# Kernel optimization log

Hardware: AMD Instinct MI355X
Metric: run time of the kernel (lower is better)

The kernel has to match this reference:

```python
import jax, jax.numpy as jnp
import numpy as np

H, DH, DM = 8, 128, 1024          # n_head, d_head, d_model (n_head*d_head == d_model)
SLEN, BSZ = 256, 64               # slen <= 256 forced by pi0[:, :l]
SCALE = 1.0 / DH ** 0.5
LN_EPS = 1e-5


def setup_inputs() -> dict:
    key = jax.random.key(0)
    k0, k1, k2, k3 = jax.random.split(key, 4)
    h = jax.random.normal(k0, (SLEN, BSZ, DM), jnp.float32)
    W_qkv = jax.random.normal(k1, (H * 4 * DH, DM), jnp.float32) * (DM ** -0.5)
    W_o = jax.random.normal(k2, (DM, H * DH), jnp.float32) * ((H * DH) ** -0.5)
    pi0 = jax.random.uniform(k3, (H, 256), jnp.float32)
    ln_gamma = jnp.ones((DM,), jnp.float32)
    ln_beta = jnp.zeros((DM,), jnp.float32)
    return {"h": h, "W_qkv": W_qkv, "W_o": W_o, "pi0": pi0,
            "ln_gamma": ln_gamma, "ln_beta": ln_beta}


def _phi(x):
    # elu(x)+1 feature map, then L1-normalize over the feature dim
    x = jax.nn.elu(x) + 1.0
    return x / jnp.sum(x, axis=-1, keepdims=True)


def _causal_linear_attn(q, k, v):
    # fast_weight_sum: out_t = sum_{s<=t} (q_t . k_s) v_s  (zero initial fast weights)
    # q,k,v: [b,h,l,d]
    l = q.shape[2]
    scores = jnp.einsum('bhld,bhsd->bhls', q, k)
    mask = jnp.tril(jnp.ones((l, l), dtype=bool))
    scores = jnp.where(mask, scores, jnp.zeros((), scores.dtype))
    return jnp.einsum('bhls,bhsd->bhld', scores, v)


def reference(h, W_qkv, W_o, pi0, ln_gamma, ln_beta):
    l, b, _ = h.shape
    # qkv projection: [l,b,H,4*DH] -> q, k1, k2, v (update_mode='rbf2keys')
    qkv = jnp.einsum('lbm,nm->lbn', h, W_qkv).reshape(l, b, H, 4 * DH)
    q, k1, k2, v = jnp.split(qkv, 4, axis=-1)
    # permute to [b, H, l, d]
    q = _phi(jnp.transpose(q, (1, 2, 0, 3)))
    k1 = _phi(jnp.transpose(k1, (1, 2, 0, 3)))
    k2 = _phi(jnp.transpose(k2, (1, 2, 0, 3)))
    v = jnp.transpose(v, (1, 2, 0, 3))
    # two fast-weight sums (skip_attn_normalization=True path)
    lo1 = _causal_linear_attn(q, k1, v)
    lo2 = _causal_linear_attn(q, k2, v)
    pi = jnp.clip(pi0, 0.0, 1.0)[None, :, :l, None]          # [1,H,l,1]
    layer_out = SCALE * (lo1 * pi + lo2 * (1.0 - pi))         # [b,H,l,d]
    # [b,H,l,d] -> [l,b,H*d]
    layer_out = jnp.transpose(layer_out, (2, 0, 1, 3)).reshape(l, b, H * DH)
    attn_out = jnp.einsum('lbn,mn->lbm', layer_out, W_o)
    # post-LN residual (pre_lnorm=False, dropout=0)
    x = h + attn_out
    mu = jnp.mean(x, axis=-1, keepdims=True)
    var = jnp.mean((x - mu) ** 2, axis=-1, keepdims=True)
    return ln_gamma * (x - mu) / jnp.sqrt(var + LN_EPS) + ln_beta
```

## Files before the change

kernel.cpp:

```cpp
#include <hip/hip_runtime.h>

#define H_     8
#define DM_    1024
#define NQKV_  4096
#define ROWS_  16384
#define PAIRS_ 512
#define SCALE_ 0.08838834764831845f
#define LN_EPS_ 1e-5f

typedef __attribute__((ext_vector_type(8))) short short8;
typedef __attribute__((ext_vector_type(4))) short short4v;
typedef __attribute__((ext_vector_type(4))) float floatx4;

__device__ __forceinline__ float b2f(unsigned short u) {
  union { unsigned int i; float f; } v; v.i = ((unsigned int)u) << 16; return v.f;
}
__device__ __forceinline__ unsigned short f2b(float f) {
  union { unsigned int i; float f; } v; v.f = f;
  unsigned int b = v.i;
  b += 0x7FFFu + ((b >> 16) & 1u);
  return (unsigned short)(b >> 16);
}

__device__ __forceinline__ void gl_lds(const unsigned short* g, unsigned short* s) {
  __builtin_amdgcn_global_load_lds(
      (const __attribute__((address_space(1))) unsigned int*)g,
      (__attribute__((address_space(3))) unsigned int*)s, 16, 0, 0);
}

__device__ __forceinline__ void stage_async(const unsigned short* __restrict__ g,
                                            size_t ld, unsigned short* s, int tid) {
#pragma unroll
  for (int p = 0; p < 4; ++p) {
    int idx = p * 256 + tid;
    int r = idx >> 3, j = idx & 7;
    int cg = j ^ (r & 7);
    gl_lds(g + (size_t)r * ld + cg * 8, s + (size_t)idx * 8);
  }
}
__device__ __forceinline__ void stage_h(const unsigned short* __restrict__ g,
                                        size_t o0, size_t o1,
                                        unsigned short* s, int lo0, int lo1) {
  gl_lds(g + o0, s + lo0);
  gl_lds(g + o1, s + lo1);
}
__device__ __forceinline__ short8 lds_frag(const unsigned short* s, int row, int cg) {
  return *(const short8*)(s + row * 64 + ((cg ^ (row & 7)) << 3));
}

__global__ __launch_bounds__(256) void cvt_all(const float* __restrict__ h,
                                               const float* __restrict__ wq,
                                               const float* __restrict__ wo,
                                               unsigned short* __restrict__ hb,
                                               unsigned short* __restrict__ wqb,
                                               unsigned short* __restrict__ wob) {
  int i = blockIdx.x * 256 + threadIdx.x;
  const float* src; unsigned short* dst; int off;
  if (i < 2097152)      { src = h;  dst = hb;  off = i; }
  else if (i < 2621440) { src = wq; dst = wqb; off = i - 2097152; }
  else                  { src = wo; dst = wob; off = i - 2621440; }
  const float4* s4 = (const float4*)(src + (size_t)off * 8);
  float4 v0 = s4[0], v1 = s4[1];
  union { short8 v; unsigned short u[8]; } pk;
  pk.u[0] = f2b(v0.x); pk.u[1] = f2b(v0.y); pk.u[2] = f2b(v0.z); pk.u[3] = f2b(v0.w);
  pk.u[4] = f2b(v1.x); pk.u[5] = f2b(v1.y); pk.u[6] = f2b(v1.z); pk.u[7] = f2b(v1.w);
  *(short8*)(dst + (size_t)off * 8) = pk.v;
}

__global__ __launch_bounds__(1024, 4) void qkv_gemm(const unsigned short* __restrict__ A,
                                                    const unsigned short* __restrict__ B,
                                                    unsigned short* __restrict__ QKV) {
  __shared__ alignas(16) unsigned short Sh[65536];
  int tid = threadIdx.x;
  int lane = tid & 63, wid = tid >> 6;
  int wm = wid >> 2, wn = wid & 3;
  int quad = lane >> 4, l16 = lane & 15;
  int s7 = l16 & 7;

  int bid = blockIdx.y * 16 + blockIdx.x;
  int swz = (bid & 7) * 128 + (bid >> 3);
  int bx = swz & 15, by = swz >> 4;
  int n0 = bx * 256, hh = bx >> 1, part0 = (bx & 1) * 2, bb = by;

  const unsigned short* AbP = A + (size_t)bb * DM_;
  const size_t lda = (size_t)64 * DM_;
  const unsigned short* BbP = B + (size_t)n0 * DM_;

  int r0 = tid >> 3, jj = tid & 7;
  int cg = jj ^ (r0 & 7);
  size_t oA = (size_t)r0 * lda + cg * 8;
  size_t oB = (size_t)r0 * DM_ + cg * 8;
  int lo = tid * 8;

  floatx4 acc[4][4];
#pragma unroll
  for (int i = 0; i < 4; ++i)
#pragma unroll
    for (int j = 0; j < 4; ++j)
#pragma unroll
      for (int r = 0; r < 4; ++r) acc[i][j][r] = 0.f;

#define QSTAGE(KT, SA)                                                         \
  gl_lds(AbP + (KT) + oA,                     (SA) + lo);                      \
  gl_lds(AbP + (KT) + oA + (size_t)128 * lda, (SA) + 8192 + lo);               \
  gl_lds(BbP + (KT) + oB,                     (SA) + 16384 + lo);              \
  gl_lds(BbP + (KT) + oB + (size_t)128 * DM_, (SA) + 24576 + lo);

  QSTAGE(0, Sh)

  for (int t = 0; t < 16; ++t) {
    unsigned short* SA = Sh + (t & 1) * 32768;
    if (t < 15) { QSTAGE((size_t)(t + 1) * 64, Sh + ((t + 1) & 1) * 32768) }
    if (t < 15) { asm volatile("s_waitcnt vmcnt(4)" ::: "memory"); }
    else        { asm volatile("s_waitcnt vmcnt(0)" ::: "memory"); }
    __builtin_amdgcn_s_barrier();
    const unsigned short* aB0 = SA + (wm * 64 + l16) * 64 + ((quad ^ s7) << 3);
    const unsigned short* aB1 = SA + (wm * 64 + l16) * 64 + (((4 + quad) ^ s7) << 3);
    const unsigned short* bB0 = SA + 16384 + (wn * 64 + l16) * 64 + ((quad ^ s7) << 3);
    const unsigned short* bB1 = SA + 16384 + (wn * 64 + l16) * 64 + (((4 + quad) ^ s7) << 3);
    short8 a[4], b[4];
#pragma unroll
    for (int mt = 0; mt < 4; ++mt) a[mt] = *(const short8*)(aB0 + mt * 1024);
#pragma unroll
    for (int nt = 0; nt < 4; ++nt) b[nt] = *(const short8*)(bB0 + nt * 1024);
#pragma unroll
    for (int mt = 0; mt < 4; ++mt)
#pragma unroll
      for (int nt = 0; nt < 4; ++nt)
        acc[mt][nt] = __builtin_amdgcn_mfma_f32_16x16x32_bf16(a[mt], b[nt], acc[mt][nt], 0, 0, 0);
#pragma unroll
    for (int mt = 0; mt < 4; ++mt) a[mt] = *(const short8*)(aB1 + mt * 1024);
#pragma unroll
    for (int nt = 0; nt < 4; ++nt) b[nt] = *(const short8*)(bB1 + nt * 1024);
#pragma unroll
    for (int mt = 0; mt < 4; ++mt)
#pragma unroll
      for (int nt = 0; nt < 4; ++nt)
        acc[mt][nt] = __builtin_amdgcn_mfma_f32_16x16x32_bf16(a[mt], b[nt], acc[mt][nt], 0, 0, 0);
    __builtin_amdgcn_s_barrier();
  }
#undef QSTAGE

  int c16 = tid & 15, g64 = tid >> 4;
  bool isV = (part0 + (wn >> 1)) == 3;
  float* Pf = (float*)Sh;
  float rsum[4][4], inv[4][4];
  if (!isV) {
#pragma unroll
    for (int mt = 0; mt < 4; ++mt)
#pragma unroll
      for (int r = 0; r < 4; ++r) rsum[mt][r] = 0.f;
#pragma unroll
    for (int mt = 0; mt < 4; ++mt)
#pragma unroll
      for (int nt = 0; nt < 4; ++nt)
#pragma unroll
        for (int r = 0; r < 4; ++r) {
          float x = acc[mt][nt][r];
          float f = x > 0.f ? x + 1.f : __expf(x);
          acc[mt][nt][r] = f;
          rsum[mt][r] += f;
        }
#pragma unroll
    for (int off = 1; off < 16; off <<= 1)
#pragma unroll
      for (int mt = 0; mt < 4; ++mt)
#pragma unroll
        for (int r = 0; r < 4; ++r)
          rsum[mt][r] += __shfl_xor(rsum[mt][r], off);
    if (l16 == 0) {
#pragma unroll
      for (int mt = 0; mt < 4; ++mt)
#pragma unroll
        for (int r = 0; r < 4; ++r)
          Pf[(wm * 64 + mt * 16 + quad * 4 + r) * 4 + wn] = rsum[mt][r];
    }
  }
  __syncthreads();
  if (!isV) {
#pragma unroll
    for (int mt = 0; mt < 4; ++mt)
#pragma unroll
      for (int r = 0; r < 4; ++r)
        inv[mt][r] = 1.f / (rsum[mt][r] + Pf[(wm * 64 + mt * 16 + quad * 4 + r) * 4 + (wn ^ 1)]);
  }
  __syncthreads();

#pragma unroll
  for (int hq = 0; hq < 2; ++hq) {
    int part = part0 + hq;
    if ((wn >> 1) == hq) {
      if (part < 3) {
#pragma unroll
        for (int mt = 0; mt < 4; ++mt)
#pragma unroll
          for (int nt = 0; nt < 4; ++nt)
#pragma unroll
            for (int r = 0; r < 4; ++r) {
              int row = wm * 64 + mt * 16 + quad * 4 + r;
              int col = (wn & 1) * 64 + nt * 16 + l16;
              Sh[row * 136 + col] = f2b(acc[mt][nt][r] * inv[mt][r]);
            }
      } else {
#pragma unroll
        for (int mt = 0; mt < 4; ++mt)
#pragma unroll
          for (int nt = 0; nt < 4; ++nt)
#pragma unroll
            for (int r = 0; r < 4; ++r) {
              int d = (wn & 1) * 64 + nt * 16 + l16;
              int l = wm * 64 + mt * 16 + quad * 4 + r;
              Sh[d * 264 + l] = f2b(acc[mt][nt][r]);
            }
      }
    }
    __syncthreads();
    if (part < 3) {
      unsigned short* P = QKV + (size_t)part * 16777216 + (size_t)(bb * 8 + hh) * 32768;
#pragma unroll
      for (int j = 0; j < 4; ++j) {
        int row = j * 64 + g64;
        *(short8*)(P + (size_t)row * 128 + c16 * 8) = *(const short8*)(Sh + row * 136 + c16 * 8);
      }
    } else {
      unsigned short* Vt = QKV + (size_t)3 * 16777216 + (size_t)(bb * 8 + hh) * 32768;
      int cg2 = tid & 31, g32 = tid >> 5;
#pragma unroll
      for (int j = 0; j < 4; ++j) {
        int d = j * 32 + g32;
        *(short8*)(Vt + (size_t)d * 256 + cg2 * 8) = *(const short8*)(Sh + d * 264 + cg2 * 8);
      }
    }
    __syncthreads();
  }
}

#define TILE_BODY(T, BUF, OBUF)                                                \
  {                                                                            \
    unsigned short* SB = (BUF) + 16384;                                        \
    const unsigned short* aA0 = (BUF) + (wm * 128 + l16) * 64 + ((quad ^ s7) << 3); \
    const unsigned short* aA1 = (BUF) + (wm * 128 + l16) * 64 + (((4 + quad) ^ s7) << 3); \
    const unsigned short* bA0 = SB + (wn * 64 + l16) * 64 + ((quad ^ s7) << 3);\
    const unsigned short* bA1 = SB + (wn * 64 + l16) * 64 + (((4 + quad) ^ s7) << 3); \
    short8 a[8], b[4];                                                         \
    if ((T) < 15) {                                                            \
      size_t kn = (size_t)((T) + 1) * 64;                                      \
      stage_h(BbP + kn,  oB0, oB1, (OBUF) + 16384, lo0, lo1);                  \
      stage_h(BbHP + kn, oB0, oB1, (OBUF) + 24576, lo0, lo1);                  \
    }                                                                          \
    _Pragma("unroll")                                                          \
    for (int mt = 0; mt < 4; ++mt) {                                           \
      a[mt * 2 + 0] = *(const short8*)(aA0 + mt * 1024);                       \
      a[mt * 2 + 1] = *(const short8*)(aA1 + mt * 1024);                       \
    }                                                                          \
    _Pragma("unroll")                                                          \
    for (int nt = 0; nt < 2; ++nt) {                                           \
      b[nt * 2 + 0] = *(const short8*)(bA0 + nt * 1024);                       \
      b[nt * 2 + 1] = *(const short8*)(bA1 + nt * 1024);                       \
    }                                                                          \
    __builtin_amdgcn_sched_barrier(0);                                         \
    __builtin_amdgcn_s_barrier();                                              \
    __builtin_amdgcn_s_setprio(1);                                             \
    _Pragma("unroll")                                                          \
    for (int kk = 0; kk < 2; ++kk)                                             \
      _Pragma("unroll")                                                        \
      for (int m = 0; m < 4; ++m)                                              \
        _Pragma("unroll")                                                      \
        for (int n = 0; n < 2; ++n)                                            \
          acc[m][n] = __builtin_amdgcn_mfma_f32_16x16x32_bf16(a[m * 2 + kk], b[n * 2 + kk], acc[m][n], 0, 0, 0); \
    __builtin_amdgcn_s_setprio(0);                                             \
    __builtin_amdgcn_s_barrier();                                              \
    _Pragma("unroll")                                                          \
    for (int nt = 0; nt < 2; ++nt) {                                           \
      b[nt * 2 + 0] = *(const short8*)(bA0 + 2048 + nt * 1024);                \
      b[nt * 2 + 1] = *(const short8*)(bA1 + 2048 + nt * 1024);                \
    }                                                                          \
    __builtin_amdgcn_sched_barrier(0);                                         \
    __builtin_amdgcn_s_barrier();                                              \
    __builtin_amdgcn_s_setprio(1);                                             \
    _Pragma("unroll")                                                          \
    for (int kk = 0; kk < 2; ++kk)                                             \
      _Pragma("unroll")                                                        \
      for (int m = 0; m < 4; ++m)                                              \
        _Pragma("unroll")                                                      \
        for (int n = 0; n < 2; ++n)                                            \
          acc[m][2 + n] = __builtin_amdgcn_mfma_f32_16x16x32_bf16(a[m * 2 + kk], b[n * 2 + kk], acc[m][2 + n], 0, 0, 0); \
    __builtin_amdgcn_s_setprio(0);                                             \
    __builtin_amdgcn_s_barrier();                                              \
    _Pragma("unroll")                                                          \
    for (int mt = 0; mt < 4; ++mt) {                                           \
      a[mt * 2 + 0] = *(const short8*)(aA0 + 4096 + mt * 1024);                \
      a[mt * 2 + 1] = *(const short8*)(aA1 + 4096 + mt * 1024);                \
    }                                                                          \
    __builtin_amdgcn_sched_barrier(0);                                         \
    __builtin_amdgcn_s_barrier();                                              \
    __builtin_amdgcn_s_setprio(1);                                             \
    _Pragma("unroll")                                                          \
    for (int kk = 0; kk < 2; ++kk)                                             \
      _Pragma("unroll")                                                        \
      for (int m = 0; m < 4; ++m)                                              \
        _Pragma("unroll")                                                      \
        for (int n = 0; n < 2; ++n)                                            \
          acc[4 + m][2 + n] = __builtin_amdgcn_mfma_f32_16x16x32_bf16(a[m * 2 + kk], b[n * 2 + kk], acc[4 + m][2 + n], 0, 0, 0); \
    __builtin_amdgcn_s_setprio(0);                                             \
    __builtin_amdgcn_s_barrier();                                              \
    if ((T) < 14) {                                                            \
      size_t kt2 = (size_t)((T) + 2) * 64;                                     \
      stage_h(AbP + kt2,  oA0, oA1, (BUF),        lo0, lo1);                   \
      stage_h(AbHP + kt2, oA0, oA1, (BUF) + 8192, lo0, lo1);                   \
    }                                                                          \
    _Pragma("unroll")                                                          \
    for (int nt = 0; nt < 2; ++nt) {                                           \
      b[nt * 2 + 0] = *(const short8*)(bA0 + nt * 1024);                       \
      b[nt * 2 + 1] = *(const short8*)(bA1 + nt * 1024);                       \
    }                                                                          \
    __builtin_amdgcn_sched_barrier(0);                                         \
    __builtin_amdgcn_s_barrier();                                              \
    __builtin_amdgcn_s_setprio(1);                                             \
    _Pragma("unroll")                                                          \
    for (int kk = 0; kk < 2; ++kk)                                             \
      _Pragma("unroll")                                                        \
      for (int m = 0; m < 4; ++m)                                              \
        _Pragma("unroll")                                                      \
        for (int n = 0; n < 2; ++n)                                            \
          acc[4 + m][n] = __builtin_amdgcn_mfma_f32_16x16x32_bf16(a[m * 2 + kk], b[n * 2 + kk], acc[4 + m][n], 0, 0, 0); \
    __builtin_amdgcn_s_setprio(0);                                             \
    if ((T) < 14) { asm volatile("s_waitcnt vmcnt(4)" ::: "memory"); }         \
    else          { asm volatile("s_waitcnt vmcnt(0)" ::: "memory"); }         \
    __builtin_amdgcn_s_barrier();                                              \
  }

__global__ __launch_bounds__(256) void scores_kernel(const unsigned short* __restrict__ QKV,
                                                     const float* __restrict__ pi0,
                                                     unsigned short* __restrict__ S) {
  __shared__ alignas(16) unsigned short Sh[24576];
  __shared__ float pis[128];
  unsigned short* As  = Sh;
  unsigned short* Bs1 = Sh + 8192;
  unsigned short* Bs2 = Sh + 16384;
  int p = blockIdx.z;
  int hh = p & 7;
  int tid = threadIdx.x;
  int lane = tid & 63, wid = tid >> 6;
  int wm = wid >> 1, wn = wid & 1;
  int quad = lane >> 4, l16 = lane & 15;
  int tix = blockIdx.x;
  int m0 = (tix >= 1) ? 128 : 0;
  int n0 = (tix == 2) ? 128 : 0;
  if (tid < 128) {
    float pv = pi0[hh * 256 + m0 + tid];
    pis[tid] = fminf(fmaxf(pv, 0.f), 1.f);
  }
  const unsigned short* Qb  = QKV + (size_t)p * 32768 + (size_t)m0 * 128;
  const unsigned short* K1b = QKV + 16777216     + (size_t)p * 32768 + (size_t)n0 * 128;
  const unsigned short* K2b = QKV + 2 * 16777216 + (size_t)p * 32768 + (size_t)n0 * 128;

  floatx4 acc1[4][4], acc2[4][4];
#pragma unroll
  for (int i = 0; i < 4; ++i)
#pragma unroll
    for (int j = 0; j < 4; ++j)
#pragma unroll
      for (int r = 0; r < 4; ++r) { acc1[i][j][r] = 0.f; acc2[i][j][r] = 0.f; }

  for (int kt = 0; kt < 128; kt += 64) {
    stage_async(Qb + kt, 128, As, tid);
    stage_async(K1b + kt, 128, Bs1, tid);
    stage_async(K2b + kt, 128, Bs2, tid);
    __syncthreads();
#pragma unroll
    for (int kk = 0; kk < 2; ++kk) {
      short8 af[4], b1[4], b2v[4];
#pragma unroll
      for (int mt = 0; mt < 4; ++mt)
        af[mt] = lds_frag(As, wm * 64 + mt * 16 + l16, kk * 4 + quad);
#pragma unroll
      for (int nt = 0; nt < 4; ++nt) {
        b1[nt]  = lds_frag(Bs1, wn * 64 + nt * 16 + l16, kk * 4 + quad);
        b2v[nt] = lds_frag(Bs2, wn * 64 + nt * 16 + l16, kk * 4 + quad);
      }
#pragma unroll
      for (int mt = 0; mt < 4; ++mt)
#pragma unroll
        for (int nt = 0; nt < 4; ++nt) {
          acc1[mt][nt] = __builtin_amdgcn_mfma_f32_16x16x32_bf16(af[mt], b1[nt],  acc1[mt][nt], 0, 0, 0);
          acc2[mt][nt] = __builtin_amdgcn_mfma_f32_16x16x32_bf16(af[mt], b2v[nt], acc2[mt][nt], 0, 0, 0);
        }
    }
    __syncthreads();
  }
#pragma unroll
  for (int mt = 0; mt < 4; ++mt)
#pragma unroll
    for (int nt = 0; nt < 4; ++nt)
#pragma unroll
      for (int r = 0; r < 4; ++r) {
        int tl = wm * 64 + mt * 16 + quad * 4 + r;
        int sl = wn * 64 + nt * 16 + l16;
        float pv = pis[tl];
        float v = (n0 + sl <= m0 + tl) ? (pv * acc1[mt][nt][r] + (1.f - pv) * acc2[mt][nt][r]) : 0.f;
        Sh[tl * 136 + sl] = f2b(v);
      }
  __syncthreads();
  int c = tid & 15, g = tid >> 4;
#pragma unroll
  for (int j = 0; j < 8; ++j) {
    int r = j * 16 + g;
    size_t gb = (size_t)p * 65536 + (size_t)(m0 + r) * 256 + n0 + c * 8;
    *(short8*)(S + gb) = *(const short8*)(Sh + r * 136 + c * 8);
  }
}

__global__ __launch_bounds__(256, 4) void pv_kernel(const unsigned short* __restrict__ S,
                                                    const unsigned short* __restrict__ Vt,
                                                    unsigned short* __restrict__ LO) {
  __shared__ alignas(16) unsigned short Sh[17408];
  unsigned short* As = Sh;
  unsigned short* Bs = Sh + 8192;
  int p = blockIdx.z;
  int b = p >> 3, hh = p & 7;
  int tid = threadIdx.x;
  int lane = tid & 63, wid = tid >> 6;
  int wm = wid >> 1, wn = wid & 1;
  int quad = lane >> 4, l16 = lane & 15;
  int m0 = blockIdx.y * 128;
  int kEnd = (blockIdx.y == 0) ? 128 : 256;
  const unsigned short* Ab = S  + (size_t)p * 65536 + (size_t)m0 * 256;
  const unsigned short* Bb = Vt + (size_t)p * 32768;

  floatx4 acc[4][4];
#pragma unroll
  for (int i = 0; i < 4; ++i)
#pragma unroll
    for (int j = 0; j < 4; ++j)
#pragma unroll
      for (int r = 0; r < 4; ++r) acc[i][j][r] = 0.f;

  for (int kt = 0; kt < kEnd; kt += 64) {
    stage_async(Ab + kt, 256, As, tid);
    stage_async(Bb + kt, 256, Bs, tid);
    __syncthreads();
#pragma unroll
    for (int kk = 0; kk < 2; ++kk) {
      short8 af[4], bfv[4];
#pragma unroll
      for (int mt = 0; mt < 4; ++mt)
        af[mt] = lds_frag(As, wm * 64 + mt * 16 + l16, kk * 4 + quad);
#pragma unroll
      for (int nt = 0; nt < 4; ++nt)
        bfv[nt] = lds_frag(Bs, wn * 64 + nt * 16 + l16, kk * 4 + quad);
#pragma unroll
      for (int mt = 0; mt < 4; ++mt)
#pragma unroll
        for (int nt = 0; nt < 4; ++nt)
          acc[mt][nt] = __builtin_amdgcn_mfma_f32_16x16x32_bf16(af[mt], bfv[nt], acc[mt][nt], 0, 0, 0);
    }
    __syncthreads();
  }
#pragma unroll
  for (int mt = 0; mt < 4; ++mt)
#pragma unroll
    for (int nt = 0; nt < 4; ++nt)
#pragma unroll
      for (int r = 0; r < 4; ++r) {
        int tl = wm * 64 + mt * 16 + quad * 4 + r;
        int d = wn * 64 + nt * 16 + l16;
        Sh[tl * 136 + d] = f2b(SCALE_ * acc[mt][nt][r]);
      }
  __syncthreads();
  int c = tid & 15, g = tid >> 4;
#pragma unroll
  for (int j = 0; j < 8; ++j) {
    int r = j * 16 + g;
    int t = m0 + r;
    size_t gb = ((size_t)t * 64 + b) * 1024 + hh * 128 + c * 8;
    *(short8*)(LO + gb) = *(const short8*)(Sh + r * 136 + c * 8);
  }
}

__global__ __launch_bounds__(512, 1) void wo_gemm(const unsigned short* __restrict__ A,
                                                  const unsigned short* __restrict__ B,
                                                  unsigned short* __restrict__ attn) {
  __shared__ alignas(16) unsigned short Sh[65536];
  int tid = threadIdx.x;
  int lane = tid & 63, wid = tid >> 6;
  int wm = wid >> 2, wn = wid & 3;
  int quad = lane >> 4, l16 = lane & 15;
  int s7 = l16 & 7;

  int bid = blockIdx.y * 4 + blockIdx.x;
  int swz = (bid & 7) * 32 + (bid >> 3);
  int bx = swz & 3, by = swz >> 2;
  int n0 = bx * 256, m0 = by * 256;

  const unsigned short* AbP = A + (size_t)m0 * DM_;
  const unsigned short* AbHP = AbP + (size_t)128 * DM_;
  const unsigned short* BbP = B + (size_t)n0 * DM_;
  const unsigned short* BbHP = BbP + (size_t)128 * DM_;

  int r0 = tid >> 3, jj = tid & 7;
  int cg = jj ^ (r0 & 7);
  size_t oA0 = (size_t)r0 * DM_ + cg * 8;
  size_t oA1 = (size_t)(r0 + 64) * DM_ + cg * 8;
  size_t oB0 = oA0, oB1 = oA1;
  int lo0 = tid * 8, lo1 = 4096 + tid * 8;

  floatx4 acc[8][4];
#pragma unroll
  for (int i = 0; i < 8; ++i)
#pragma unroll
    for (int j = 0; j < 4; ++j)
#pragma unroll
      for (int r = 0; r < 4; ++r) acc[i][j][r] = 0.f;

  stage_h(AbP,        oA0, oA1, Sh,         lo0, lo1);
  stage_h(AbHP,       oA0, oA1, Sh + 8192,  lo0, lo1);
  stage_h(BbP,        oB0, oB1, Sh + 16384, lo0, lo1);
  stage_h(BbHP,       oB0, oB1, Sh + 24576, lo0, lo1);
  stage_h(AbP + 64,   oA0, oA1, Sh + 32768, lo0, lo1);
  stage_h(AbHP + 64,  oA0, oA1, Sh + 40960, lo0, lo1);
  asm volatile("s_waitcnt vmcnt(4)" ::: "memory");
  __builtin_amdgcn_s_barrier();

  for (int t = 0; t < 16; t += 2) {
    TILE_BODY(t,     Sh,         Sh + 32768)
    TILE_BODY(t + 1, Sh + 32768, Sh)
  }

  __syncthreads();
#pragma unroll
  for (int hq = 0; hq < 2; ++hq) {
    if ((wn >> 1) == hq) {
#pragma unroll
      for (int mt = 0; mt < 8; ++mt)
#pragma unroll
        for (int nt = 0; nt < 4; ++nt)
#pragma unroll
          for (int r = 0; r < 4; ++r) {
            int row = wm * 128 + mt * 16 + quad * 4 + r;
            int col = (wn & 1) * 64 + nt * 16 + l16;
            Sh[row * 136 + col] = f2b(acc[mt][nt][r]);
          }
    }
    __syncthreads();
    int c = tid & 15, g = tid >> 4;
#pragma unroll
    for (int j = 0; j < 8; ++j) {
      int row = j * 32 + g;
      *(short8*)(attn + (size_t)(m0 + row) * DM_ + n0 + hq * 128 + c * 8) =
          *(const short8*)(Sh + row * 136 + c * 8);
    }
    __syncthreads();
  }
}

__global__ __launch_bounds__(256) void ln_res(const unsigned short* __restrict__ attn,
                                              const float* __restrict__ hin,
                                              const float* __restrict__ gamma,
                                              const float* __restrict__ beta,
                                              float* __restrict__ out) {
  int row = blockIdx.x;
  int tid = threadIdx.x;
  const unsigned short* ap = attn + (size_t)row * DM_ + tid * 4;
  const float* hp = hin + (size_t)row * DM_ + tid * 4;
  short4v av = *(const short4v*)ap;
  float4 hv = *(const float4*)hp;
  float x[4];
  x[0] = hv.x + b2f((unsigned short)av[0]);
  x[1] = hv.y + b2f((unsigned short)av[1]);
  x[2] = hv.z + b2f((unsigned short)av[2]);
  x[3] = hv.w + b2f((unsigned short)av[3]);
  float s  = x[0] + x[1] + x[2] + x[3];
  float ss = x[0] * x[0] + x[1] * x[1] + x[2] * x[2] + x[3] * x[3];
#pragma unroll
  for (int off = 32; off; off >>= 1) {
    s  += __shfl_down(s, off);
    ss += __shfl_down(ss, off);
  }
  __shared__ float rs[4], rss[4];
  int wv = tid >> 6, lane = tid & 63;
  if (lane == 0) { rs[wv] = s; rss[wv] = ss; }
  __syncthreads();
  float St  = rs[0] + rs[1] + rs[2] + rs[3];
  float SSt = rss[0] + rss[1] + rss[2] + rss[3];
  float mu = St * (1.f / DM_);
  float var = SSt * (1.f / DM_) - mu * mu;
  float rstd = rsqrtf(var + LN_EPS_);
  float4 o;
#pragma unroll
  for (int j = 0; j < 4; ++j) {
    int c = tid * 4 + j;
    (&o.x)[j] = gamma[c] * (x[j] - mu) * rstd + beta[c];
  }
  *(float4*)(out + (size_t)row * DM_ + tid * 4) = o;
}

extern "C" void kernel_launch(void* const* d_in, const int* in_sizes, int n_in,
                              void* d_out, int out_size, void* d_ws, size_t ws_size,
                              hipStream_t stream) {
  const float* h     = (const float*)d_in[0];
  const float* Wqkv  = (const float*)d_in[1];
  const float* Wo    = (const float*)d_in[2];
  const float* pi0   = (const float*)d_in[3];
  const float* gamma = (const float*)d_in[4];
  const float* beta  = (const float*)d_in[5];
  char* ws = (char*)d_ws;

  unsigned short* QKV   = (unsigned short*)ws;
  unsigned short* Sbuf  = (unsigned short*)(ws + 134217728ull);
  unsigned short* hb    = (unsigned short*)(ws + 134217728ull);
  unsigned short* Wqkvb = (unsigned short*)(ws + 167772160ull);
  unsigned short* Wob   = (unsigned short*)(ws + 201326592ull);
  unsigned short* LO    = (unsigned short*)ws;
  unsigned short* attn  = (unsigned short*)(ws + 134217728ull);
  float* X = (float*)d_out;

  dim3 blk(256);
  cvt_all<<<dim3(10752), blk, 0, stream>>>(h, Wqkv, Wo, hb, Wqkvb, Wob);
  qkv_gemm<<<dim3(16, 64, 1), dim3(1024), 0, stream>>>(hb, Wqkvb, QKV);
  scores_kernel<<<dim3(3, 1, PAIRS_), blk, 0, stream>>>(QKV, pi0, Sbuf);
  pv_kernel<<<dim3(1, 2, PAIRS_), blk, 0, stream>>>(Sbuf, QKV + (size_t)3 * 16777216, LO);
  wo_gemm<<<dim3(4, 64, 1), dim3(512), 0, stream>>>(LO, Wob, attn);
  ln_res<<<dim3(ROWS_, 1, 1), blk, 0, stream>>>(attn, h, gamma, beta, X);
}
```

Baseline: 419.7 us.

## Restructure wo_gemm to 16 warps with simpler double-buffered K loop

The output-projection GEMM goes from 8 warps, each holding a 128x64 accumulator tile, to 16 warps each holding 64x64. The hand-scheduled ping-pong TILE_BODY macro with setprio and split staging is replaced by a plain double-buffered loop that stages the next K tile, waits, and runs 32 MFMAs per warp. The aim is more wave-level parallelism and lower register pressure per thread to hide latency. The cost is losing the fine-grained interleaving of LDS reads, barriers and MFMA priority, and each LDS fragment is now reused across fewer MFMAs.

```diff
diff --git a/kernel.cpp b/kernel.cpp
--- a/kernel.cpp
+++ b/kernel.cpp
@@ -37,12 +37,6 @@
     int cg = j ^ (r & 7);
     gl_lds(g + (size_t)r * ld + cg * 8, s + (size_t)idx * 8);
   }
-}
-__device__ __forceinline__ void stage_h(const unsigned short* __restrict__ g,
-                                        size_t o0, size_t o1,
-                                        unsigned short* s, int lo0, int lo1) {
-  gl_lds(g + o0, s + lo0);
-  gl_lds(g + o1, s + lo1);
 }
 __device__ __forceinline__ short8 lds_frag(const unsigned short* s, int row, int cg) {
   return *(const short8*)(s + row * 64 + ((cg ^ (row & 7)) << 3));
@@ -234,101 +228,6 @@
     __syncthreads();
   }
 }
-
-#define TILE_BODY(T, BUF, OBUF)                                                \
-  {                                                                            \
-    unsigned short* SB = (BUF) + 16384;                                        \
-    const unsigned short* aA0 = (BUF) + (wm * 128 + l16) * 64 + ((quad ^ s7) << 3); \
-    const unsigned short* aA1 = (BUF) + (wm * 128 + l16) * 64 + (((4 + quad) ^ s7) << 3); \
-    const unsigned short* bA0 = SB + (wn * 64 + l16) * 64 + ((quad ^ s7) << 3);\
-    const unsigned short* bA1 = SB + (wn * 64 + l16) * 64 + (((4 + quad) ^ s7) << 3); \
-    short8 a[8], b[4];                                                         \
-    if ((T) < 15) {                                                            \
-      size_t kn = (size_t)((T) + 1) * 64;                                      \
-      stage_h(BbP + kn,  oB0, oB1, (OBUF) + 16384, lo0, lo1);                  \
-      stage_h(BbHP + kn, oB0, oB1, (OBUF) + 24576, lo0, lo1);                  \
-    }                                                                          \
-    _Pragma("unroll")                                                          \
-    for (int mt = 0; mt < 4; ++mt) {                                           \
-      a[mt * 2 + 0] = *(const short8*)(aA0 + mt * 1024);                       \
-      a[mt * 2 + 1] = *(const short8*)(aA1 + mt * 1024);                       \
-    }                                                                          \
-    _Pragma("unroll")                                                          \
-    for (int nt = 0; nt < 2; ++nt) {                                           \
-      b[nt * 2 + 0] = *(const short8*)(bA0 + nt * 1024);                       \
-      b[nt * 2 + 1] = *(const short8*)(bA1 + nt * 1024);                       \
-    }                                                                          \
-    __builtin_amdgcn_sched_barrier(0);                                         \
-    __builtin_amdgcn_s_barrier();                                              \
-    __builtin_amdgcn_s_setprio(1);                                             \
-    _Pragma("unroll")                                                          \
-    for (int kk = 0; kk < 2; ++kk)                                             \
-      _Pragma("unroll")                                                        \
-      for (int m = 0; m < 4; ++m)                                              \
-        _Pragma("unroll")                                                      \
-        for (int n = 0; n < 2; ++n)                                            \
-          acc[m][n] = __builtin_amdgcn_mfma_f32_16x16x32_bf16(a[m * 2 + kk], b[n * 2 + kk], acc[m][n], 0, 0, 0); \
-    __builtin_amdgcn_s_setprio(0);                                             \
-    __builtin_amdgcn_s_barrier();                                              \
-    _Pragma("unroll")                                                          \
-    for (int nt = 0; nt < 2; ++nt) {                                           \
-      b[nt * 2 + 0] = *(const short8*)(bA0 + 2048 + nt * 1024);                \
-      b[nt * 2 + 1] = *(const short8*)(bA1 + 2048 + nt * 1024);                \
-    }                                                                          \
-    __builtin_amdgcn_sched_barrier(0);                                         \
-    __builtin_amdgcn_s_barrier();                                              \
-    __builtin_amdgcn_s_setprio(1);                                             \
-    _Pragma("unroll")                                                          \
-    for (int kk = 0; kk < 2; ++kk)                                             \
-      _Pragma("unroll")                                                        \
-      for (int m = 0; m < 4; ++m)                                              \
-        _Pragma("unroll")                                                      \
-        for (int n = 0; n < 2; ++n)                                            \
-          acc[m][2 + n] = __builtin_amdgcn_mfma_f32_16x16x32_bf16(a[m * 2 + kk], b[n * 2 + kk], acc[m][2 + n], 0, 0, 0); \
-    __builtin_amdgcn_s_setprio(0);                                             \
-    __builtin_amdgcn_s_barrier();                                              \
-    _Pragma("unroll")                                                          \
-    for (int mt = 0; mt < 4; ++mt) {                                           \
-      a[mt * 2 + 0] = *(const short8*)(aA0 + 4096 + mt * 1024);                \
-      a[mt * 2 + 1] = *(const short8*)(aA1 + 4096 + mt * 1024);                \
-    }                                                                          \
-    __builtin_amdgcn_sched_barrier(0);                                         \
-    __builtin_amdgcn_s_barrier();                                              \
-    __builtin_amdgcn_s_setprio(1);                                             \
-    _Pragma("unroll")                                                          \
-    for (int kk = 0; kk < 2; ++kk)                                             \
-      _Pragma("unroll")                                                        \
-      for (int m = 0; m < 4; ++m)                                              \
-        _Pragma("unroll")                                                      \
-        for (int n = 0; n < 2; ++n)                                            \
-          acc[4 + m][2 + n] = __builtin_amdgcn_mfma_f32_16x16x32_bf16(a[m * 2 + kk], b[n * 2 + kk], acc[4 + m][2 + n], 0, 0, 0); \
-    __builtin_amdgcn_s_setprio(0);                                             \
-    __builtin_amdgcn_s_barrier();                                              \
-    if ((T) < 14) {                                                            \
-      size_t kt2 = (size_t)((T) + 2) * 64;                                     \
-      stage_h(AbP + kt2,  oA0, oA1, (BUF),        lo0, lo1);                   \
-      stage_h(AbHP + kt2, oA0, oA1, (BUF) + 8192, lo0, lo1);                   \
-    }                                                                          \
-    _Pragma("unroll")                                                          \
-    for (int nt = 0; nt < 2; ++nt) {                                           \
-      b[nt * 2 + 0] = *(const short8*)(bA0 + nt * 1024);                       \
-      b[nt * 2 + 1] = *(const short8*)(bA1 + nt * 1024);                       \
-    }                                                                          \
-    __builtin_amdgcn_sched_barrier(0);                                         \
-    __builtin_amdgcn_s_barrier();                                              \
-    __builtin_amdgcn_s_setprio(1);                                             \
-    _Pragma("unroll")                                                          \
-    for (int kk = 0; kk < 2; ++kk)                                             \
-      _Pragma("unroll")                                                        \
-      for (int m = 0; m < 4; ++m)                                              \
-        _Pragma("unroll")                                                      \
-        for (int n = 0; n < 2; ++n)                                            \
-          acc[4 + m][n] = __builtin_amdgcn_mfma_f32_16x16x32_bf16(a[m * 2 + kk], b[n * 2 + kk], acc[4 + m][n], 0, 0, 0); \
-    __builtin_amdgcn_s_setprio(0);                                             \
-    if ((T) < 14) { asm volatile("s_waitcnt vmcnt(4)" ::: "memory"); }         \
-    else          { asm volatile("s_waitcnt vmcnt(0)" ::: "memory"); }         \
-    __builtin_amdgcn_s_barrier();                                              \
-  }
 
 __global__ __launch_bounds__(256) void scores_kernel(const unsigned short* __restrict__ QKV,
                                                      const float* __restrict__ pi0,
@@ -478,9 +377,9 @@
   }
 }
 
-__global__ __launch_bounds__(512, 1) void wo_gemm(const unsigned short* __restrict__ A,
-                                                  const unsigned short* __restrict__ B,
-                                                  unsigned short* __restrict__ attn) {
+__global__ __launch_bounds__(1024, 4) void wo_gemm(const unsigned short* __restrict__ A,
+                                                   const unsigned short* __restrict__ B,
+                                                   unsigned short* __restrict__ attn) {
   __shared__ alignas(16) unsigned short Sh[65536];
   int tid = threadIdx.x;
   int lane = tid & 63, wid = tid >> 6;
@@ -494,61 +393,84 @@
   int n0 = bx * 256, m0 = by * 256;
 
   const unsigned short* AbP = A + (size_t)m0 * DM_;
-  const unsigned short* AbHP = AbP + (size_t)128 * DM_;
   const unsigned short* BbP = B + (size_t)n0 * DM_;
-  const unsigned short* BbHP = BbP + (size_t)128 * DM_;
 
   int r0 = tid >> 3, jj = tid & 7;
   int cg = jj ^ (r0 & 7);
-  size_t oA0 = (size_t)r0 * DM_ + cg * 8;
-  size_t oA1 = (size_t)(r0 + 64) * DM_ + cg * 8;
-  size_t oB0 = oA0, oB1 = oA1;
-  int lo0 = tid * 8, lo1 = 4096 + tid * 8;
-
-  floatx4 acc[8][4];
-#pragma unroll
-  for (int i = 0; i < 8; ++i)
+  size_t oA = (size_t)r0 * DM_ + cg * 8;
+  int lo = tid * 8;
+
+  floatx4 acc[4][4];
+#pragma unroll
+  for (int i = 0; i < 4; ++i)
 #pragma unroll
     for (int j = 0; j < 4; ++j)
 #pragma unroll
       for (int r = 0; r < 4; ++r) acc[i][j][r] = 0.f;
 
-  stage_h(AbP,        oA0, oA1, Sh,         lo0, lo1);
-  stage_h(AbHP,       oA0, oA1, Sh + 8192,  lo0, lo1);
-  stage_h(BbP,        oB0, oB1, Sh + 16384, lo0, lo1);
-  stage_h(BbHP,       oB0, oB1, Sh + 24576, lo0, lo1);
-  stage_h(AbP + 64,   oA0, oA1, Sh + 32768, lo0, lo1);
-  stage_h(AbHP + 64,  oA0, oA1, Sh + 40960, lo0, lo1);
-  asm volatile("s_waitcnt vmcnt(4)" ::: "memory");
-  __builtin_amdgcn_s_barrier();
-
-  for (int t = 0; t < 16; t += 2) {
-    TILE_BODY(t,     Sh,         Sh + 32768)
-    TILE_BODY(t + 1, Sh + 32768, Sh)
-  }
+#define WSTAGE(KT, SA)                                                         \
+  gl_lds(AbP + (KT) + oA,                     (SA) + lo);                      \
+  gl_lds(AbP + (KT) + oA + (size_t)128 * DM_, (SA) + 8192 + lo);               \
+  gl_lds(BbP + (KT) + oA,                     (SA) + 16384 + lo);              \
+  gl_lds(BbP + (KT) + oA + (size_t)128 * DM_, (SA) + 24576 + lo);
+
+  WSTAGE(0, Sh)
+
+  for (int t = 0; t < 16; ++t) {
+    unsigned short* SA = Sh + (t & 1) * 32768;
+    if (t < 15) { WSTAGE((size_t)(t + 1) * 64, Sh + ((t + 1) & 1) * 32768) }
+    if (t < 15) { asm volatile("s_waitcnt vmcnt(4)" ::: "memory"); }
+    else        { asm volatile("s_waitcnt vmcnt(0)" ::: "memory"); }
+    __builtin_amdgcn_s_barrier();
+    const unsigned short* aB0 = SA + (wm * 64 + l16) * 64 + ((quad ^ s7) << 3);
+    const unsigned short* aB1 = SA + (wm * 64 + l16) * 64 + (((4 + quad) ^ s7) << 3);
+    const unsigned short* bB0 = SA + 16384 + (wn * 64 + l16) * 64 + ((quad ^ s7) << 3);
+    const unsigned short* bB1 = SA + 16384 + (wn * 64 + l16) * 64 + (((4 + quad) ^ s7) << 3);
+    short8 a[4], b[4];
+#pragma unroll
+    for (int mt = 0; mt < 4; ++mt) a[mt] = *(const short8*)(aB0 + mt * 1024);
+#pragma unroll
+    for (int nt = 0; nt < 4; ++nt) b[nt] = *(const short8*)(bB0 + nt * 1024);
+#pragma unroll
+    for (int mt = 0; mt < 4; ++mt)
+#pragma unroll
+      for (int nt = 0; nt < 4; ++nt)
+        acc[mt][nt] = __builtin_amdgcn_mfma_f32_16x16x32_bf16(a[mt], b[nt], acc[mt][nt], 0, 0, 0);
+#pragma unroll
+    for (int mt = 0; mt < 4; ++mt) a[mt] = *(const short8*)(aB1 + mt * 1024);
+#pragma unroll
+    for (int nt = 0; nt < 4; ++nt) b[nt] = *(const short8*)(bB1 + nt * 1024);
+#pragma unroll
+    for (int mt = 0; mt < 4; ++mt)
+#pragma unroll
+      for (int nt = 0; nt < 4; ++nt)
+        acc[mt][nt] = __builtin_amdgcn_mfma_f32_16x16x32_bf16(a[mt], b[nt], acc[mt][nt], 0, 0, 0);
+    __builtin_amdgcn_s_barrier();
+  }
+#undef WSTAGE
 
   __syncthreads();
+  int c16 = tid & 15, g64 = tid >> 4;
 #pragma unroll
   for (int hq = 0; hq < 2; ++hq) {
     if ((wn >> 1) == hq) {
 #pragma unroll
-      for (int mt = 0; mt < 8; ++mt)
+      for (int mt = 0; mt < 4; ++mt)
 #pragma unroll
         for (int nt = 0; nt < 4; ++nt)
 #pragma unroll
           for (int r = 0; r < 4; ++r) {
-            int row = wm * 128 + mt * 16 + quad * 4 + r;
+            int row = wm * 64 + mt * 16 + quad * 4 + r;
             int col = (wn & 1) * 64 + nt * 16 + l16;
             Sh[row * 136 + col] = f2b(acc[mt][nt][r]);
           }
     }
     __syncthreads();
-    int c = tid & 15, g = tid >> 4;
-#pragma unroll
-    for (int j = 0; j < 8; ++j) {
-      int row = j * 32 + g;
-      *(short8*)(attn + (size_t)(m0 + row) * DM_ + n0 + hq * 128 + c * 8) =
-          *(const short8*)(Sh + row * 136 + c * 8);
+#pragma unroll
+    for (int j = 0; j < 4; ++j) {
+      int row = j * 64 + g64;
+      *(short8*)(attn + (size_t)(m0 + row) * DM_ + n0 + hq * 128 + c16 * 8) =
+          *(const short8*)(Sh + row * 136 + c16 * 8);
     }
     __syncthreads();
   }
@@ -620,6 +542,6 @@
   qkv_gemm<<<dim3(16, 64, 1), dim3(1024), 0, stream>>>(hb, Wqkvb, QKV);
   scores_kernel<<<dim3(3, 1, PAIRS_), blk, 0, stream>>>(QKV, pi0, Sbuf);
   pv_kernel<<<dim3(1, 2, PAIRS_), blk, 0, stream>>>(Sbuf, QKV + (size_t)3 * 16777216, LO);
-  wo_gemm<<<dim3(4, 64, 1), dim3(512), 0, stream>>>(LO, Wob, attn);
+  wo_gemm<<<dim3(4, 64, 1), dim3(1024), 0, stream>>>(LO, Wob, attn);
   ln_res<<<dim3(ROWS_, 1, 1), blk, 0, stream>>>(attn, h, gamma, beta, X);
 }
```

After: 418.5 us. About the same (-0.3%).
